# Kernel tuning notes

Measured on AMD Instinct MI355X. Metric: run time of the kernel, lower is better.

Reference implementation:

```python
import jax, jax.numpy as jnp
import numpy as np
from jax import lax

T_LOW, T_HIGH = 100.0, 200.0   # init kwargs of Canny
TG22 = 0.4142135623730951      # tan(22.5 deg), cv2's direction quantization constant
MAX_ITERS = 512                # safety cap on hysteresis fixed-point loop


def _shift(a, dy, dx):
    # neighbor value n[y, x] = a[y + dy, x + dx], zero outside
    H, W = a.shape
    p = jnp.pad(a, 1)
    return p[1 + dy:1 + dy + H, 1 + dx:1 + dx + W]


def _canny(x):
    B, C, H, W = x.shape
    # toRGB: ((x+1)/2*255).to(uint8)  (truncation; values are non-negative)
    img = jnp.clip(jnp.floor((x + 1.0) * 0.5 * 255.0), 0.0, 255.0)
    # original reshapes batch into one tall strip (B*H, W, C) before cv2.Canny
    img = img.transpose(0, 2, 3, 1).reshape(B * H, W, C)
    HH = B * H
    p = jnp.pad(img, ((1, 1), (1, 1), (0, 0)), mode='edge')  # replicate border like cv2

    def s(dy, dx):
        return p[1 + dy:1 + dy + HH, 1 + dx:1 + dx + W, :]

    # 3x3 Sobel per channel
    gx = (s(-1, 1) + 2.0 * s(0, 1) + s(1, 1)) - (s(-1, -1) + 2.0 * s(0, -1) + s(1, -1))
    gy = (s(1, -1) + 2.0 * s(1, 0) + s(1, 1)) - (s(-1, -1) + 2.0 * s(-1, 0) + s(-1, 1))
    mag_c = jnp.abs(gx) + jnp.abs(gy)  # L1 magnitude (cv2 default L2gradient=False)
    # multi-channel: take channel with max magnitude per pixel (cv2 behavior)
    idx = jnp.argmax(mag_c, axis=-1, keepdims=True)
    gx = jnp.take_along_axis(gx, idx, -1)[..., 0]
    gy = jnp.take_along_axis(gy, idx, -1)[..., 0]
    mag = jnp.take_along_axis(mag_c, idx, -1)[..., 0]

    # non-maximum suppression with 4 quantized directions
    ax_, ay_ = jnp.abs(gx), jnp.abs(gy)
    is_h = ay_ < TG22 * ax_          # gradient ~horizontal -> compare left/right
    is_v = ay_ * TG22 > ax_          # gradient ~vertical -> compare up/down
    same = (gx * gy) >= 0.0          # diagonal orientation by sign agreement
    n1 = jnp.where(is_h, _shift(mag, 0, -1),
         jnp.where(is_v, _shift(mag, -1, 0),
         jnp.where(same, _shift(mag, -1, -1), _shift(mag, -1, 1))))
    n2 = jnp.where(is_h, _shift(mag, 0, 1),
         jnp.where(is_v, _shift(mag, 1, 0),
         jnp.where(same, _shift(mag, 1, 1), _shift(mag, 1, -1))))
    keep = (mag > n1) & (mag >= n2)

    strong = keep & (mag > T_HIGH)
    weak = keep & (mag > T_LOW)

    # hysteresis: propagate strong labels through 8-connected weak pixels to fixed point
    def dilate(m):
        mf = m.astype(jnp.float32)
        return lax.reduce_window(mf, 0.0, lax.add, (3, 3), (1, 1), 'SAME') > 0.0

    def body(st):
        s0, _, it = st
        grown = (dilate(s0) & weak) | s0
        return grown, jnp.any(grown != s0), it + 1

    def cond(st):
        return st[1] & (st[2] < MAX_ITERS)

    strong, _, _ = lax.while_loop(cond, body, (strong, jnp.array(True), jnp.array(0)))

    edges = strong.reshape(B, H, W).astype(jnp.float32)        # {0,1} == cv2 {0,255}/255
    edges = jnp.broadcast_to(edges[:, None, :, :], (B, 3, H, W))
    return (edges - 0.5) / 0.5                                 # T.Normalize(0.5, 0.5)


def setup_inputs() -> dict:
    key = jax.random.key(0)
    x = jax.random.uniform(key, (16, 3, 512, 512), jnp.float32, -1.0, 1.0)
    return {"x": x}


def reference(x):
    return _canny(x)
```

## Files before the change

### kernel.cpp

```cpp
#include <hip/hip_runtime.h>
#include <stdint.h>

#define HH 8192
#define WW 512
#define WPR 8
#define TG22F 0.4142135623730951f
#define NSWEEP 6


__device__ __forceinline__ float to_img(float v) {
    float t = floorf((v + 1.0f) * 0.5f * 255.0f);
    return fminf(fmaxf(t, 0.0f), 255.0f);
}

__device__ __forceinline__ int bsel(uint64_t w0, uint64_t w1, int idx) {
    return (idx < 8) ? (int)((w0 >> (idx * 8)) & 255)
                     : (int)((w1 >> ((idx - 8) * 8)) & 255);
}

__device__ __forceinline__ uint64_t runfill(uint64_t s, uint64_t w) {
    uint64_t sw = s & w;
    uint64_t up = ((sw + w) ^ w) & w;
    uint64_t rs = __brevll(sw);
    uint64_t rw = __brevll(w);
    uint64_t dn = __brevll(((rs + rw) ^ rw) & rw);
    return up | dn | sw;
}

__device__ __forceinline__ uint64_t shfl_up64(uint64_t v, int d) {
    int lo = __shfl_up((int)(uint32_t)v, d, 64);
    int hi = __shfl_up((int)(uint32_t)(v >> 32), d, 64);
    return ((uint64_t)(uint32_t)hi << 32) | (uint32_t)lo;
}
__device__ __forceinline__ uint64_t shfl_dn64(uint64_t v, int d) {
    int lo = __shfl_down((int)(uint32_t)v, d, 64);
    int hi = __shfl_down((int)(uint32_t)(v >> 32), d, 64);
    return ((uint64_t)(uint32_t)hi << 32) | (uint32_t)lo;
}

__global__ void k_sobel(const float* __restrict__ in, uint16_t* __restrict__ packed) {
    __shared__ uint8_t simg[3 * 34 * 72];
    const int tid = threadIdx.x;
    const int row0 = (blockIdx.x >> 3) << 5;
    const int col0 = (blockIdx.x & 7) << 6;

    for (int i = tid; i < 1632; i += 256) {
        int c = i / 544;
        int rem = i - c * 544;
        int hr = rem >> 4;
        int q = rem & 15;
        int gy = row0 + hr - 1;
        gy = gy < 0 ? 0 : (gy >= HH ? HH - 1 : gy);
        int b = gy >> 9, h = gy & 511;
        const float4 v = *(const float4*)&in[((((b * 3 + c) << 9) + h) << 9) + col0 + (q << 2)];
        uint32_t pk = (uint32_t)(uint8_t)to_img(v.x)
                    | ((uint32_t)(uint8_t)to_img(v.y) << 8)
                    | ((uint32_t)(uint8_t)to_img(v.z) << 16)
                    | ((uint32_t)(uint8_t)to_img(v.w) << 24);
        *(uint32_t*)&simg[(c * 34 + hr) * 72 + 4 + (q << 2)] = pk;
    }
    for (int i = tid; i < 204; i += 256) {
        int c = i / 68;
        int rem = i - c * 68;
        int hr = rem >> 1;
        int side = rem & 1;
        int gy = row0 + hr - 1;
        gy = gy < 0 ? 0 : (gy >= HH ? HH - 1 : gy);
        int gc = side ? col0 + 64 : col0 - 1;
        gc = gc < 0 ? 0 : (gc >= WW ? WW - 1 : gc);
        int b = gy >> 9, h = gy & 511;
        float v = to_img(in[((((b * 3 + c) << 9) + h) << 9) + gc]);
        simg[(c * 34 + hr) * 72 + (side ? 68 : 3)] = (uint8_t)v;
    }
    __syncthreads();

    const int r = tid >> 3;
    const int c8 = (tid & 7) << 3;

    int bestMag[8], bgx[8], bgy[8];
    #pragma unroll
    for (int j = 0; j < 8; ++j) { bestMag[j] = -1; bgx[j] = 0; bgy[j] = 0; }

    #pragma unroll
    for (int c = 0; c < 3; ++c) {
        const uint8_t* base = &simg[(c * 34 + r) * 72 + c8];
        uint64_t w00 = *(const uint64_t*)(base);
        uint64_t w01 = *(const uint64_t*)(base + 8);
        uint64_t w10 = *(const uint64_t*)(base + 72);
        uint64_t w11 = *(const uint64_t*)(base + 80);
        uint64_t w20 = *(const uint64_t*)(base + 144);
        uint64_t w21 = *(const uint64_t*)(base + 152);
        int vs[10], t0[10], t2[10];
        #pragma unroll
        for (int i = 0; i < 10; ++i) {
            int a0 = bsel(w00, w01, 3 + i);
            int a1 = bsel(w10, w11, 3 + i);
            int a2 = bsel(w20, w21, 3 + i);
            vs[i] = a0 + 2 * a1 + a2;
            t0[i] = a0; t2[i] = a2;
        }
        #pragma unroll
        for (int j = 0; j < 8; ++j) {
            int gx = vs[j + 2] - vs[j];
            int gy = (t2[j] + 2 * t2[j + 1] + t2[j + 2]) - (t0[j] + 2 * t0[j + 1] + t0[j + 2]);
            int mg = abs(gx) + abs(gy);
            if (mg > bestMag[j]) { bestMag[j] = mg; bgx[j] = gx; bgy[j] = gy; }
        }
    }

    uint32_t res[4];
    #pragma unroll
    for (int jj = 0; jj < 4; ++jj) {
        uint32_t pair = 0;
        #pragma unroll
        for (int s = 0; s < 2; ++s) {
            int j = jj * 2 + s;
            float axf = (float)abs(bgx[j]);
            float ayf = (float)abs(bgy[j]);
            int dir;
            if (ayf < TG22F * axf)      dir = 0;
            else if (ayf * TG22F > axf) dir = 1;
            else                        dir = (bgx[j] * bgy[j] >= 0) ? 2 : 3;
            uint32_t val = (uint32_t)(bestMag[j] | (dir << 12));
            pair |= val << (s * 16);
        }
        res[jj] = pair;
    }
    int y = row0 + r;
    *(uint4*)&packed[y * WW + col0 + c8] = *(uint4*)res;
}

__global__ void k_nms(const uint16_t* __restrict__ packed,
                      unsigned long long* __restrict__ strongB,
                      unsigned long long* __restrict__ weakB,
                      int* __restrict__ flags) {
    if (blockIdx.x == 0 && threadIdx.x < 16) flags[threadIdx.x] = 0;
    int y = blockIdx.x >> 1;
    int x = ((blockIdx.x & 1) << 8) + threadIdx.x;
    uint16_t own = packed[y * WW + x];
    int mag = own & 0xFFF;
    int dir = own >> 12;
    int d1y = (dir == 0) ? 0 : -1;
    int d1x = (dir == 0) ? -1 : (dir == 1) ? 0 : (dir == 2) ? -1 : 1;
    int n1y = y + d1y, n1x = x + d1x;
    int n2y = y - d1y, n2x = x - d1x;
    int n1 = (n1y >= 0 && n1y < HH && n1x >= 0 && n1x < WW) ? (packed[n1y * WW + n1x] & 0xFFF) : 0;
    int n2 = (n2y >= 0 && n2y < HH && n2x >= 0 && n2x < WW) ? (packed[n2y * WW + n2x] & 0xFFF) : 0;
    bool keep = (mag > n1) && (mag >= n2);
    bool strong = keep && (mag > 200);
    bool weak   = keep && (mag > 100);
    unsigned long long sb = __ballot(strong ? 1 : 0);
    unsigned long long wb = __ballot(weak ? 1 : 0);
    if ((threadIdx.x & 63) == 0) {
        int word = y * WPR + (x >> 6);
        strongB[word] = sb;
        weakB[word]   = wb;
    }
}

__global__ void __launch_bounds__(256) k_wsweep(
        const unsigned long long* __restrict__ weakB,
        unsigned long long* __restrict__ buf,
        int* __restrict__ flags, int sidx)
{
    if (sidx > 0 && flags[sidx - 1] == 0) return;
    const int lane = threadIdx.x & 63;
    const int wave = (blockIdx.x << 2) + (threadIdx.x >> 6);
    const int base = ((wave << 6) + lane) * WPR;

    uint64_t own[8], wk[8];
    #pragma unroll
    for (int k = 0; k < 8; ++k) { wk[k] = weakB[base + k]; own[k] = buf[base + k]; }

    uint64_t hu[8], hd[8];
    #pragma unroll
    for (int k = 0; k < 8; ++k) { hu[k] = 0; hd[k] = 0; }
    if (lane == 0 && wave > 0) {
        #pragma unroll
        for (int k = 0; k < 8; ++k) hu[k] = buf[base - WPR + k];
    }
    if (lane == 63 && wave < 127) {
        #pragma unroll
        for (int k = 0; k < 8; ++k) hd[k] = buf[base + WPR + k];
    }
    uint64_t hspu[8], hspd[8];
    #pragma unroll
    for (int k = 0; k < 8; ++k) {
        uint64_t a = hu[k] | (hu[k] << 1) | (hu[k] >> 1);
        if (k > 0) a |= hu[k - 1] >> 63;
        if (k < 7) a |= hu[k + 1] << 63;
        hspu[k] = a;
        uint64_t b = hd[k] | (hd[k] << 1) | (hd[k] >> 1);
        if (k > 0) b |= hd[k - 1] >> 63;
        if (k < 7) b |= hd[k + 1] << 63;
        hspd[k] = b;
    }

    bool grew = false;
    for (;;) {
        uint64_t sp[8];
        #pragma unroll
        for (int k = 0; k < 8; ++k) {
            uint64_t h = own[k] | (own[k] << 1) | (own[k] >> 1);
            if (k > 0) h |= own[k - 1] >> 63;
            if (k < 7) h |= own[k + 1] << 63;
            sp[k] = h;
        }
        uint64_t su[8], sd[8];
        #pragma unroll
        for (int k = 0; k < 8; ++k) {
            su[k] = shfl_up64(sp[k], 1);
            sd[k] = shfl_dn64(sp[k], 1);
        }
        if (lane == 0) {
            #pragma unroll
            for (int k = 0; k < 8; ++k) su[k] = hspu[k];
        }
        if (lane == 63) {
            #pragma unroll
            for (int k = 0; k < 8; ++k) sd[k] = hspd[k];
        }
        uint32_t ch = 0;
        #pragma unroll
        for (int k = 0; k < 8; ++k) {
            uint64_t acc = sp[k] | su[k] | sd[k];
            uint64_t nv = runfill(own[k] | (acc & wk[k]), wk[k]);
            ch |= (uint32_t)(nv != own[k]);
            own[k] = nv;
        }
        if (ch) grew = true;
        if (__ballot(ch ? 1 : 0) == 0ull) break;
    }

    if (__ballot(grew ? 1 : 0) != 0ull) {
        #pragma unroll
        for (int k = 0; k < 8; ++k) buf[base + k] = own[k];
        if (lane == 0)
            __hip_atomic_store(&flags[sidx], 1, __ATOMIC_RELAXED, __HIP_MEMORY_SCOPE_AGENT);
    }
}

__global__ void k_out(const unsigned long long* __restrict__ result, float* __restrict__ out) {
    int t = blockIdx.x * blockDim.x + threadIdx.x;
    int b = t >> 16;
    int r = t & 65535;
    int h = r >> 7;
    int w = (r & 127) << 2;
    int y = (b << 9) + h;
    unsigned long long word = result[y * WPR + (w >> 6)];
    int sh = w & 63;
    float4 v;
    v.x = ((word >> (sh + 0)) & 1ull) ? 1.0f : -1.0f;
    v.y = ((word >> (sh + 1)) & 1ull) ? 1.0f : -1.0f;
    v.z = ((word >> (sh + 2)) & 1ull) ? 1.0f : -1.0f;
    v.w = ((word >> (sh + 3)) & 1ull) ? 1.0f : -1.0f;
    int base = (b * 3) << 18;
    int off = (h << 9) + w;
    *(float4*)&out[base + off] = v;
    *(float4*)&out[base + 262144 + off] = v;
    *(float4*)&out[base + 524288 + off] = v;
}

extern "C" void kernel_launch(void* const* d_in, const int* in_sizes, int n_in,
                              void* d_out, int out_size, void* d_ws, size_t ws_size,
                              hipStream_t stream) {
    const float* x = (const float*)d_in[0];
    float* out = (float*)d_out;
    char* ws = (char*)d_ws;

    uint16_t* packed          = (uint16_t*)(ws);
    unsigned long long* buf   = (unsigned long long*)(ws + 8388608);
    unsigned long long* weakB = (unsigned long long*)(ws + 8912896);
    int* flags                = (int*)(ws + 9437184);

    k_sobel<<<2048, 256, 0, stream>>>(x, packed);
    k_nms<<<HH * 2, 256, 0, stream>>>(packed, buf, weakB, flags);
    for (int s = 0; s < NSWEEP; ++s)
        k_wsweep<<<32, 256, 0, stream>>>(weakB, buf, flags, s);
    k_out<<<4096, 256, 0, stream>>>(buf, out);
}
```

Before: 137.1 us.

## Fuse hysteresis sweep launches into one persistent kernel with grid barriers

Replaces the sequence of separate hysteresis sweep kernel launches with a single 32-block persistent kernel. Each round does a wave-local fixed-point fill, then publishes its boundary rows and meets the other blocks at an atomic-counter grid barrier before reloading halos. It exits early once a round shows no growth anywhere. This removes per-launch overhead and avoids reloading full state each sweep, but it relies on all 32 blocks being co-resident and on the barrier counters in flags[8..15] starting at zero. It also raises the round cap from 6 to 8.

New measurement: 132.2 us. -3.5%, faster.

```diff
diff --git a/kernel.cpp b/kernel.cpp
--- a/kernel.cpp
+++ b/kernel.cpp
@@ -5,7 +5,8 @@
 #define WW 512
 #define WPR 8
 #define TG22F 0.4142135623730951f
-#define NSWEEP 6
+#define NROUND 8
+#define NBLK 32
 
 
 __device__ __forceinline__ float to_img(float v) {
@@ -158,12 +159,11 @@
     }
 }
 
-__global__ void __launch_bounds__(256) k_wsweep(
+__global__ void __launch_bounds__(256) k_hyst(
         const unsigned long long* __restrict__ weakB,
         unsigned long long* __restrict__ buf,
-        int* __restrict__ flags, int sidx)
+        int* __restrict__ flags)
 {
-    if (sidx > 0 && flags[sidx - 1] == 0) return;
     const int lane = threadIdx.x & 63;
     const int wave = (blockIdx.x << 2) + (threadIdx.x >> 6);
     const int base = ((wave << 6) + lane) * WPR;
@@ -172,71 +172,100 @@
     #pragma unroll
     for (int k = 0; k < 8; ++k) { wk[k] = weakB[base + k]; own[k] = buf[base + k]; }
 
-    uint64_t hu[8], hd[8];
-    #pragma unroll
-    for (int k = 0; k < 8; ++k) { hu[k] = 0; hd[k] = 0; }
-    if (lane == 0 && wave > 0) {
-        #pragma unroll
-        for (int k = 0; k < 8; ++k) hu[k] = buf[base - WPR + k];
-    }
-    if (lane == 63 && wave < 127) {
-        #pragma unroll
-        for (int k = 0; k < 8; ++k) hd[k] = buf[base + WPR + k];
-    }
     uint64_t hspu[8], hspd[8];
     #pragma unroll
-    for (int k = 0; k < 8; ++k) {
-        uint64_t a = hu[k] | (hu[k] << 1) | (hu[k] >> 1);
-        if (k > 0) a |= hu[k - 1] >> 63;
-        if (k < 7) a |= hu[k + 1] << 63;
-        hspu[k] = a;
-        uint64_t b = hd[k] | (hd[k] << 1) | (hd[k] >> 1);
-        if (k > 0) b |= hd[k - 1] >> 63;
-        if (k < 7) b |= hd[k + 1] << 63;
-        hspd[k] = b;
-    }
-
-    bool grew = false;
-    for (;;) {
-        uint64_t sp[8];
-        #pragma unroll
-        for (int k = 0; k < 8; ++k) {
-            uint64_t h = own[k] | (own[k] << 1) | (own[k] >> 1);
-            if (k > 0) h |= own[k - 1] >> 63;
-            if (k < 7) h |= own[k + 1] << 63;
-            sp[k] = h;
-        }
-        uint64_t su[8], sd[8];
-        #pragma unroll
-        for (int k = 0; k < 8; ++k) {
-            su[k] = shfl_up64(sp[k], 1);
-            sd[k] = shfl_dn64(sp[k], 1);
-        }
-        if (lane == 0) {
-            #pragma unroll
-            for (int k = 0; k < 8; ++k) su[k] = hspu[k];
-        }
-        if (lane == 63) {
-            #pragma unroll
-            for (int k = 0; k < 8; ++k) sd[k] = hspd[k];
-        }
-        uint32_t ch = 0;
-        #pragma unroll
-        for (int k = 0; k < 8; ++k) {
-            uint64_t acc = sp[k] | su[k] | sd[k];
-            uint64_t nv = runfill(own[k] | (acc & wk[k]), wk[k]);
-            ch |= (uint32_t)(nv != own[k]);
-            own[k] = nv;
-        }
-        if (ch) grew = true;
-        if (__ballot(ch ? 1 : 0) == 0ull) break;
-    }
-
-    if (__ballot(grew ? 1 : 0) != 0ull) {
+    for (int k = 0; k < 8; ++k) { hspu[k] = 0; hspd[k] = 0; }
+
+    auto load_halo = [&]() {
+        uint64_t h[8];
+        if (lane == 0 && wave > 0) {
+            #pragma unroll
+            for (int k = 0; k < 8; ++k) h[k] = buf[base - WPR + k];
+            #pragma unroll
+            for (int k = 0; k < 8; ++k) {
+                uint64_t a = h[k] | (h[k] << 1) | (h[k] >> 1);
+                if (k > 0) a |= h[k - 1] >> 63;
+                if (k < 7) a |= h[k + 1] << 63;
+                hspu[k] = a;
+            }
+        }
+        if (lane == 63 && wave < 127) {
+            #pragma unroll
+            for (int k = 0; k < 8; ++k) h[k] = buf[base + WPR + k];
+            #pragma unroll
+            for (int k = 0; k < 8; ++k) {
+                uint64_t a = h[k] | (h[k] << 1) | (h[k] >> 1);
+                if (k > 0) a |= h[k - 1] >> 63;
+                if (k < 7) a |= h[k + 1] << 63;
+                hspd[k] = a;
+            }
+        }
+    };
+    load_halo();
+
+    bool grewAny = false;
+    for (int r = 0; r < NROUND; ++r) {
+        bool grew = false;
+        for (;;) {
+            uint64_t sp[8];
+            #pragma unroll
+            for (int k = 0; k < 8; ++k) {
+                uint64_t h = own[k] | (own[k] << 1) | (own[k] >> 1);
+                if (k > 0) h |= own[k - 1] >> 63;
+                if (k < 7) h |= own[k + 1] << 63;
+                sp[k] = h;
+            }
+            uint64_t su[8], sd[8];
+            #pragma unroll
+            for (int k = 0; k < 8; ++k) {
+                su[k] = shfl_up64(sp[k], 1);
+                sd[k] = shfl_dn64(sp[k], 1);
+            }
+            if (lane == 0) {
+                #pragma unroll
+                for (int k = 0; k < 8; ++k) su[k] = hspu[k];
+            }
+            if (lane == 63) {
+                #pragma unroll
+                for (int k = 0; k < 8; ++k) sd[k] = hspd[k];
+            }
+            uint32_t ch = 0;
+            #pragma unroll
+            for (int k = 0; k < 8; ++k) {
+                uint64_t acc = sp[k] | su[k] | sd[k];
+                uint64_t nv = runfill(own[k] | (acc & wk[k]), wk[k]);
+                ch |= (uint32_t)(nv != own[k]);
+                own[k] = nv;
+            }
+            if (ch) grew = true;
+            if (__ballot(ch ? 1 : 0) == 0ull) break;
+        }
+        grewAny |= grew;
+
+        if (grew && lane == 0)
+            __hip_atomic_store(&flags[r], 1, __ATOMIC_RELAXED, __HIP_MEMORY_SCOPE_AGENT);
+        if (lane == 0 || lane == 63) {
+            #pragma unroll
+            for (int k = 0; k < 8; ++k) buf[base + k] = own[k];
+        }
+        __syncthreads();
+        if (threadIdx.x == 0) {
+            __threadfence();
+            __hip_atomic_fetch_add(&flags[8 + r], 1, __ATOMIC_ACQ_REL, __HIP_MEMORY_SCOPE_AGENT);
+            while (__hip_atomic_load(&flags[8 + r], __ATOMIC_ACQUIRE, __HIP_MEMORY_SCOPE_AGENT) < NBLK)
+                __builtin_amdgcn_s_sleep(1);
+            __threadfence();
+        }
+        __syncthreads();
+
+        if (__hip_atomic_load(&flags[r], __ATOMIC_RELAXED, __HIP_MEMORY_SCOPE_AGENT) == 0)
+            break;
+        if (r + 1 < NROUND) load_halo();
+    }
+
+    if (__ballot(grewAny ? 1 : 0) != 0ull) {
         #pragma unroll
         for (int k = 0; k < 8; ++k) buf[base + k] = own[k];
-        if (lane == 0)
-            __hip_atomic_store(&flags[sidx], 1, __ATOMIC_RELAXED, __HIP_MEMORY_SCOPE_AGENT);
     }
 }
 
@@ -275,7 +304,6 @@
 
     k_sobel<<<2048, 256, 0, stream>>>(x, packed);
     k_nms<<<HH * 2, 256, 0, stream>>>(packed, buf, weakB, flags);
-    for (int s = 0; s < NSWEEP; ++s)
-        k_wsweep<<<32, 256, 0, stream>>>(weakB, buf, flags, s);
+    k_hyst<<<NBLK, 256, 0, stream>>>(weakB, buf, flags);
     k_out<<<4096, 256, 0, stream>>>(buf, out);
 }
```
